# Kernel optimization log

Measured on AMD Instinct MI355X. Metric: run time of the kernel, lower is better.

Reference implementation:

```python
import jax, jax.numpy as jnp
import numpy as np

N = 50000      # nodes
E = 800000     # edges (avg degree 16)
B = 250        # graphs in batch
T = 8          # temporal slices
CIN = 32
COUT = 64


def setup_inputs() -> dict:
    key = jax.random.key(0)
    ks = jax.random.split(key, 9)
    x = jax.random.normal(ks[0], (N, CIN, T), dtype=jnp.float32)
    edge_index = jax.random.randint(ks[1], (2, E), 0, N, dtype=jnp.int64)
    # 250 graphs of 200 nodes each -> every segment non-empty (safe for segment_max)
    batch = jnp.repeat(jnp.arange(B, dtype=jnp.int64), N // B)
    W1 = jax.random.normal(ks[2], (CIN, COUT), jnp.float32) / np.sqrt(CIN).astype(np.float32)
    b1 = jax.random.normal(ks[3], (COUT,), jnp.float32) * 0.01
    W2 = jax.random.normal(ks[4], (COUT, COUT), jnp.float32) / np.sqrt(COUT).astype(np.float32)
    b2 = jax.random.normal(ks[5], (COUT,), jnp.float32) * 0.01
    W3 = jax.random.normal(ks[6], (COUT, COUT), jnp.float32) / np.sqrt(COUT).astype(np.float32)
    b3 = jax.random.normal(ks[7], (COUT,), jnp.float32) * 0.01
    return {"x": x, "edge_index": edge_index, "batch": batch,
            "W1": W1, "b1": b1, "W2": W2, "b2": b2, "W3": W3, "b3": b3}


def reference(x, edge_index, batch, W1, b1, W2, b2, W3, b3):
    # GCNConv (PyG default): add self-loops, symmetric D^{-1/2}(A+I)D^{-1/2} norm,
    # linear transform then gather-scale-scatter aggregation, plus bias.
    src, dst = edge_index[0], edge_index[1]
    loops = jnp.arange(N, dtype=src.dtype)
    src2 = jnp.concatenate([src, loops])
    dst2 = jnp.concatenate([dst, loops])
    deg = jax.ops.segment_sum(jnp.ones_like(src2, x.dtype), dst2, num_segments=N)
    dinv = jax.lax.rsqrt(deg)  # deg >= 1 due to self-loops
    norm = dinv[src2] * dinv[dst2]  # [E+N]
    counts = jax.ops.segment_sum(jnp.ones((N,), x.dtype), batch, num_segments=B)

    def gcn(h, W, b):
        h = h @ W                              # [N, COUT]
        msg = norm[:, None] * h[src2]          # [E+N, COUT] gather + scale
        return jax.ops.segment_sum(msg, dst2, num_segments=N) + b

    def pool(h):  # cat(global_max_pool, global_mean_pool) -> [B, 2*COUT]
        mx = jax.ops.segment_max(h, batch, num_segments=B)
        mn = jax.ops.segment_sum(h, batch, num_segments=B) / counts[:, None]
        return jnp.concatenate([mx, mn], axis=1)

    def step(carry, xt):  # xt: [N, CIN]
        h1 = jax.nn.relu(gcn(xt, W1, b1))
        h2 = jax.nn.relu(gcn(h1, W2, b2))
        h3 = jax.nn.relu(gcn(h2, W3, b3))
        return carry, pool(h1) + pool(h2) + pool(h3)

    _, outs = jax.lax.scan(step, None, jnp.moveaxis(x, 2, 0))  # [T, B, 2*COUT]
    return jnp.moveaxis(outs, 0, 2)  # [B, 2*COUT, T]
```

## Files before the change

### kernel.cpp

```cpp
#include <hip/hip_runtime.h>
#include <hip/hip_fp16.h>
#include <math.h>

#define NN 50000
#define EE 800000
#define BB 250
#define TT 8
#define CIN 32
#define COUT 64
#define NPG 200
#define SCAN_B 256
#define NBLK 196
#define GC (BB * COUT)

__device__ __forceinline__ float unpack_w(unsigned int v) {
    union { unsigned short u; __half h; } cv;
    cv.u = (unsigned short)(v >> 16);
    return __half2float(cv.h);
}


__global__ void init_deg(int* deg, int* cursor) {
    int n = blockIdx.x * 256 + threadIdx.x;
    if (n < NN) { deg[n] = 1; cursor[n] = 0; }
}

__global__ void count_deg(const int* dst, int* deg) {
    int e = blockIdx.x * 256 + threadIdx.x;
    if (e < EE) atomicAdd(&deg[dst[e]], 1);
}

__global__ void compute_dinv(const int* deg, float* dinv) {
    int n = blockIdx.x * 256 + threadIdx.x;
    if (n < NN) dinv[n] = rsqrtf((float)deg[n]);
}

__global__ void scan_blocks(const int* deg, int* off, int* bsum) {
    __shared__ int sh[SCAN_B];
    int gid = blockIdx.x * SCAN_B + threadIdx.x;
    int v = (gid < NN) ? (deg[gid] - 1) : 0;
    sh[threadIdx.x] = v;
    __syncthreads();
    for (int s = 1; s < SCAN_B; s <<= 1) {
        int add = (threadIdx.x >= s) ? sh[threadIdx.x - s] : 0;
        __syncthreads();
        sh[threadIdx.x] += add;
        __syncthreads();
    }
    if (gid < NN) off[gid] = sh[threadIdx.x] - v;
    if (threadIdx.x == SCAN_B - 1) bsum[blockIdx.x] = sh[threadIdx.x];
}

__global__ void scan_sums(int* bsum, int* off) {
    __shared__ int sh[SCAN_B];
    int v = (threadIdx.x < NBLK) ? bsum[threadIdx.x] : 0;
    sh[threadIdx.x] = v;
    __syncthreads();
    for (int s = 1; s < SCAN_B; s <<= 1) {
        int add = (threadIdx.x >= s) ? sh[threadIdx.x - s] : 0;
        __syncthreads();
        sh[threadIdx.x] += add;
        __syncthreads();
    }
    if (threadIdx.x < NBLK) bsum[threadIdx.x] = sh[threadIdx.x] - v;
    if (threadIdx.x == 0) off[NN] = EE;
}

__global__ void scan_add(int* off, const int* bsum) {
    int gid = blockIdx.x * SCAN_B + threadIdx.x;
    if (gid < NN) off[gid] += bsum[blockIdx.x];
}

__global__ void fill_csr(const int* src, const int* dst, const int* off,
                         int* cursor, const float* dinv, unsigned int* csrp) {
    int e = blockIdx.x * 256 + threadIdx.x;
    if (e >= EE) return;
    int s = src[e], d = dst[e];
    int p = atomicAdd(&cursor[d], 1);
    union { __half h; unsigned short u; } cv;
    cv.h = __float2half(dinv[s] * dinv[d]);
    csrp[off[d] + p] = (unsigned int)s | ((unsigned int)cv.u << 16);
}

__global__ void scratch_init(float* scr, int ntot) {
    int i = blockIdx.x * 256 + threadIdx.x;
    if (i < ntot) scr[i] = 0.f;
}


__global__ void agg_x_allT16(const float* __restrict__ x, const int* __restrict__ off,
                             const unsigned int* __restrict__ csrp,
                             const float* __restrict__ dinv, __half2* __restrict__ xa2) {
    int lane = threadIdx.x & 63;
    int w = threadIdx.x >> 6;
    int n = blockIdx.x * 4 + w;
    float dn = dinv[n];
    float sw = dn * dn;
    float4 v = ((const float4*)(x + (size_t)n * 256))[lane];
    float4 acc = make_float4(sw * v.x, sw * v.y, sw * v.z, sw * v.w);
    int e0 = off[n], e1 = off[n + 1];
    for (int base = e0; base < e1; base += 64) {
        int idx = base + lane;
        unsigned int cme = (idx < e1) ? csrp[idx] : 0u;
        int cnt = min(64, e1 - base);
        int k = 0;
        for (; k + 7 < cnt; k += 8) {
            unsigned int p0 = __shfl(cme, k, 64),     p1 = __shfl(cme, k + 1, 64);
            unsigned int p2 = __shfl(cme, k + 2, 64), p3 = __shfl(cme, k + 3, 64);
            unsigned int p4 = __shfl(cme, k + 4, 64), p5 = __shfl(cme, k + 5, 64);
            unsigned int p6 = __shfl(cme, k + 6, 64), p7 = __shfl(cme, k + 7, 64);
            float4 u0 = ((const float4*)(x + (size_t)(p0 & 0xffff) * 256))[lane];
            float4 u1 = ((const float4*)(x + (size_t)(p1 & 0xffff) * 256))[lane];
            float4 u2 = ((const float4*)(x + (size_t)(p2 & 0xffff) * 256))[lane];
            float4 u3 = ((const float4*)(x + (size_t)(p3 & 0xffff) * 256))[lane];
            float4 u4 = ((const float4*)(x + (size_t)(p4 & 0xffff) * 256))[lane];
            float4 u5 = ((const float4*)(x + (size_t)(p5 & 0xffff) * 256))[lane];
            float4 u6 = ((const float4*)(x + (size_t)(p6 & 0xffff) * 256))[lane];
            float4 u7 = ((const float4*)(x + (size_t)(p7 & 0xffff) * 256))[lane];
            float w0 = unpack_w(p0), w1 = unpack_w(p1), w2 = unpack_w(p2), w3 = unpack_w(p3);
            float w4 = unpack_w(p4), w5 = unpack_w(p5), w6 = unpack_w(p6), w7 = unpack_w(p7);
            acc.x = fmaf(w0, u0.x, acc.x); acc.y = fmaf(w0, u0.y, acc.y);
            acc.z = fmaf(w0, u0.z, acc.z); acc.w = fmaf(w0, u0.w, acc.w);
            acc.x = fmaf(w1, u1.x, acc.x); acc.y = fmaf(w1, u1.y, acc.y);
            acc.z = fmaf(w1, u1.z, acc.z); acc.w = fmaf(w1, u1.w, acc.w);
            acc.x = fmaf(w2, u2.x, acc.x); acc.y = fmaf(w2, u2.y, acc.y);
            acc.z = fmaf(w2, u2.z, acc.z); acc.w = fmaf(w2, u2.w, acc.w);
            acc.x = fmaf(w3, u3.x, acc.x); acc.y = fmaf(w3, u3.y, acc.y);
            acc.z = fmaf(w3, u3.z, acc.z); acc.w = fmaf(w3, u3.w, acc.w);
            acc.x = fmaf(w4, u4.x, acc.x); acc.y = fmaf(w4, u4.y, acc.y);
            acc.z = fmaf(w4, u4.z, acc.z); acc.w = fmaf(w4, u4.w, acc.w);
            acc.x = fmaf(w5, u5.x, acc.x); acc.y = fmaf(w5, u5.y, acc.y);
            acc.z = fmaf(w5, u5.z, acc.z); acc.w = fmaf(w5, u5.w, acc.w);
            acc.x = fmaf(w6, u6.x, acc.x); acc.y = fmaf(w6, u6.y, acc.y);
            acc.z = fmaf(w6, u6.z, acc.z); acc.w = fmaf(w6, u6.w, acc.w);
            acc.x = fmaf(w7, u7.x, acc.x); acc.y = fmaf(w7, u7.y, acc.y);
            acc.z = fmaf(w7, u7.z, acc.z); acc.w = fmaf(w7, u7.w, acc.w);
        }
        for (; k < cnt; ++k) {
            unsigned int p = __shfl(cme, k, 64);
            float wj = unpack_w(p);
            float4 u = ((const float4*)(x + (size_t)(p & 0xffff) * 256))[lane];
            acc.x = fmaf(wj, u.x, acc.x); acc.y = fmaf(wj, u.y, acc.y);
            acc.z = fmaf(wj, u.z, acc.z); acc.w = fmaf(wj, u.w, acc.w);
        }
    }
    __shared__ float sh[4][TT][33];
    float av[4] = {acc.x, acc.y, acc.z, acc.w};
    #pragma unroll
    for (int k = 0; k < 4; ++k) {
        int f = 4 * lane + k;
        sh[w][f & 7][f >> 3] = av[k];
    }
    __syncthreads();
    for (int i = threadIdx.x; i < 512; i += 256) {
        int t = i >> 6;
        int r = i & 63;
        int nl = r >> 4;
        int pp = r & 15;
        xa2[((size_t)(t >> 1) * NN + blockIdx.x * 4 + nl) * 32 + (t & 1) * 16 + pp] =
            __floats2half2_rn(sh[nl][t][2 * pp], sh[nl][t][2 * pp + 1]);
    }
}

__global__ void l1mat2i(const __half2* __restrict__ xa, const float* __restrict__ W1,
                        const float* __restrict__ b1, const float* __restrict__ W2,
                        __half2* __restrict__ H1,
                        float* __restrict__ pmax, float* __restrict__ psum) {
    __shared__ float W1s[CIN * COUT];
    __shared__ __half2 W2s[COUT * 32];
    __shared__ float Xs[4][2][CIN];
    __shared__ float tile[4][2][COUT];
    for (int i = threadIdx.x; i < CIN * COUT; i += 256) W1s[i] = W1[i];
    for (int i = threadIdx.x; i < COUT * 32; i += 256) {
        int k = i >> 5, pr = i & 31;
        W2s[i] = __floats2half2_rn(W2[k * COUT + 2 * pr], W2[k * COUT + 2 * pr + 1]);
    }
    if (threadIdx.x < 128) {
        int nl = threadIdx.x >> 5, idx = threadIdx.x & 31;
        int tc = idx >> 4, pp = idx & 15;
        float2 v = __half22float2(xa[((size_t)blockIdx.x * 4 + nl) * 32 + idx]);
        Xs[nl][tc][2 * pp] = v.x;
        Xs[nl][tc][2 * pp + 1] = v.y;
    }
    __syncthreads();
    int co = threadIdx.x & 63;
    int nl = threadIdx.x >> 6;
    float a0 = b1[co], a1 = b1[co];
    #pragma unroll
    for (int k = 0; k < CIN; ++k) {
        float wv = W1s[k * COUT + co];
        a0 = fmaf(Xs[nl][0][k], wv, a0);
        a1 = fmaf(Xs[nl][1][k], wv, a1);
    }
    tile[nl][0][co] = fmaxf(a0, 0.f);
    tile[nl][1][co] = fmaxf(a1, 0.f);
    __syncthreads();
    if (threadIdx.x < 128) {
        int c = threadIdx.x & 63, tc = threadIdx.x >> 6;
        float m = fmaxf(fmaxf(tile[0][tc][c], tile[1][tc][c]),
                        fmaxf(tile[2][tc][c], tile[3][tc][c]));
        float s = tile[0][tc][c] + tile[1][tc][c] + tile[2][tc][c] + tile[3][tc][c];
        int g = blockIdx.x / 50;
        atomicMax((int*)&pmax[tc * GC + g * COUT + c], __float_as_int(m));
        atomicAdd(&psum[tc * GC + g * COUT + c], s);
    }
    {
        int row = threadIdx.x >> 5;
        int pr = threadIdx.x & 31;
        int nl2 = row >> 1, tc2 = row & 1;
        float b0 = 0.f, bb1 = 0.f;
        #pragma unroll
        for (int k = 0; k < COUT; ++k) {
            float xv = tile[nl2][tc2][k];
            float2 wv = __half22float2(W2s[k * 32 + pr]);
            b0 = fmaf(xv, wv.x, b0);
            bb1 = fmaf(xv, wv.y, bb1);
        }
        H1[((size_t)blockIdx.x * 4 + nl2) * 64 + tc2 * 32 + pr] =
            __floats2half2_rn(b0, bb1);
    }
}

template <int FUSE>
__global__ void agg2i(const __half2* __restrict__ Hin, const int* __restrict__ off,
                      const unsigned int* __restrict__ csrp,
                      const float* __restrict__ dinv, const float* __restrict__ b,
                      const float* __restrict__ W, __half2* __restrict__ Hout,
                      float* __restrict__ pmax, float* __restrict__ psum) {
    __shared__ __half2 Ws[FUSE ? COUT * 32 : 1];
    __shared__ float tile[4][2][COUT];
    if (FUSE)
        for (int i = threadIdx.x; i < COUT * 32; i += 256) {
            int k = i >> 5, pr = i & 31;
            Ws[i] = __floats2half2_rn(W[k * COUT + 2 * pr], W[k * COUT + 2 * pr + 1]);
        }
    int lane = threadIdx.x & 63;
    int tc = lane >> 5;
    int p = lane & 31;
    int w = threadIdx.x >> 6;
    int n = blockIdx.x * 4 + w;
    int e0 = off[n], e1 = off[n + 1];
    float ax = 0.f, ay = 0.f;
    for (int base = e0; base < e1; base += 64) {
        int idx = base + lane;
        unsigned int cme = (idx < e1) ? csrp[idx] : 0u;
        int cnt = min(64, e1 - base);
        int k = 0;
        for (; k + 7 < cnt; k += 8) {
            unsigned int c0 = __shfl(cme, k, 64),     c1 = __shfl(cme, k + 1, 64);
            unsigned int c2 = __shfl(cme, k + 2, 64), c3 = __shfl(cme, k + 3, 64);
            unsigned int c4 = __shfl(cme, k + 4, 64), c5 = __shfl(cme, k + 5, 64);
            unsigned int c6 = __shfl(cme, k + 6, 64), c7 = __shfl(cme, k + 7, 64);
            float2 v0 = __half22float2(Hin[(size_t)(c0 & 0xffff) * 64 + lane]);
            float2 v1 = __half22float2(Hin[(size_t)(c1 & 0xffff) * 64 + lane]);
            float2 v2 = __half22float2(Hin[(size_t)(c2 & 0xffff) * 64 + lane]);
            float2 v3 = __half22float2(Hin[(size_t)(c3 & 0xffff) * 64 + lane]);
            float2 v4 = __half22float2(Hin[(size_t)(c4 & 0xffff) * 64 + lane]);
            float2 v5 = __half22float2(Hin[(size_t)(c5 & 0xffff) * 64 + lane]);
            float2 v6 = __half22float2(Hin[(size_t)(c6 & 0xffff) * 64 + lane]);
            float2 v7 = __half22float2(Hin[(size_t)(c7 & 0xffff) * 64 + lane]);
            float w0 = unpack_w(c0), w1 = unpack_w(c1), w2 = unpack_w(c2), w3 = unpack_w(c3);
            float w4 = unpack_w(c4), w5 = unpack_w(c5), w6 = unpack_w(c6), w7 = unpack_w(c7);
            ax = fmaf(w0, v0.x, ax); ay = fmaf(w0, v0.y, ay);
            ax = fmaf(w1, v1.x, ax); ay = fmaf(w1, v1.y, ay);
            ax = fmaf(w2, v2.x, ax); ay = fmaf(w2, v2.y, ay);
            ax = fmaf(w3, v3.x, ax); ay = fmaf(w3, v3.y, ay);
            ax = fmaf(w4, v4.x, ax); ay = fmaf(w4, v4.y, ay);
            ax = fmaf(w5, v5.x, ax); ay = fmaf(w5, v5.y, ay);
            ax = fmaf(w6, v6.x, ax); ay = fmaf(w6, v6.y, ay);
            ax = fmaf(w7, v7.x, ax); ay = fmaf(w7, v7.y, ay);
        }
        for (; k < cnt; ++k) {
            unsigned int c = __shfl(cme, k, 64);
            float wv = unpack_w(c);
            float2 v = __half22float2(Hin[(size_t)(c & 0xffff) * 64 + lane]);
            ax = fmaf(wv, v.x, ax); ay = fmaf(wv, v.y, ay);
        }
    }
    {
        float dn = dinv[n];
        float sw = dn * dn;
        float2 sv = __half22float2(Hin[(size_t)n * 64 + lane]);
        float ox = fmaxf(fmaf(sw, sv.x, ax) + b[2 * p], 0.f);
        float oy = fmaxf(fmaf(sw, sv.y, ay) + b[2 * p + 1], 0.f);
        tile[w][tc][2 * p] = ox;
        tile[w][tc][2 * p + 1] = oy;
    }
    __syncthreads();
    if (threadIdx.x < 128) {
        int c = threadIdx.x & 63, tcc = threadIdx.x >> 6;
        float m = fmaxf(fmaxf(tile[0][tcc][c], tile[1][tcc][c]),
                        fmaxf(tile[2][tcc][c], tile[3][tcc][c]));
        float s = tile[0][tcc][c] + tile[1][tcc][c] + tile[2][tcc][c] + tile[3][tcc][c];
        int g = blockIdx.x / 50;
        atomicMax((int*)&pmax[tcc * GC + g * COUT + c], __float_as_int(m));
        atomicAdd(&psum[tcc * GC + g * COUT + c], s);
    }
    if (FUSE) {
        int row = threadIdx.x >> 5;
        int pr = threadIdx.x & 31;
        int nl2 = row >> 1, tc2 = row & 1;
        float b0 = 0.f, bb1 = 0.f;
        #pragma unroll
        for (int k = 0; k < COUT; ++k) {
            float xv = tile[nl2][tc2][k];
            float2 wv = __half22float2(Ws[k * 32 + pr]);
            b0 = fmaf(xv, wv.x, b0);
            bb1 = fmaf(xv, wv.y, bb1);
        }
        Hout[((size_t)blockIdx.x * 4 + nl2) * 64 + tc2 * 32 + pr] =
            __floats2half2_rn(b0, bb1);
    }
}

__global__ void fold2(float* __restrict__ pmaxT, float* __restrict__ psumT,
                      float* __restrict__ out, int t0) {
    int i = blockIdx.x * 256 + threadIdx.x;
    if (i >= 2 * GC) return;
    int tc = i / GC;
    int r = i - tc * GC;
    int g = r >> 6, c = r & 63;
    float m = pmaxT[tc * GC + r] + pmaxT[2 * GC + tc * GC + r] +
              pmaxT[4 * GC + tc * GC + r];
    float mean = psumT[i] * (1.0f / NPG);
    int t = t0 + tc;
    out[((size_t)g * 128 + c) * TT + t] = m;
    out[((size_t)g * 128 + 64 + c) * TT + t] = mean;
    pmaxT[tc * GC + r] = 0.f;
    pmaxT[2 * GC + tc * GC + r] = 0.f;
    pmaxT[4 * GC + tc * GC + r] = 0.f;
    psumT[i] = 0.f;
}


extern "C" void kernel_launch(void* const* d_in, const int* in_sizes, int n_in,
                              void* d_out, int out_size, void* d_ws, size_t ws_size,
                              hipStream_t stream) {
    const float* x   = (const float*)d_in[0];
    const int*   ei  = (const int*)d_in[1];
    const int*   src = ei;
    const int*   dst = ei + EE;
    const float* W1  = (const float*)d_in[3];
    const float* b1  = (const float*)d_in[4];
    const float* W2  = (const float*)d_in[5];
    const float* b2  = (const float*)d_in[6];
    const float* W3  = (const float*)d_in[7];
    const float* b3  = (const float*)d_in[8];
    float* out = (float*)d_out;

    char* wsp = (char*)d_ws;
    auto alloc = [&](size_t bytes) {
        char* p = wsp;
        wsp += (bytes + 255) & ~(size_t)255;
        return p;
    };
    const size_t chunkHalf2 = (size_t)NN * 32;
    float*        dinv = (float*)       alloc((size_t)NN * 4);
    int*          off  = (int*)         alloc((size_t)(NN + 1) * 4);
    unsigned int* csrp = (unsigned int*)alloc((size_t)EE * 4);
    __half2*      H1   = (__half2*)     alloc((size_t)NN * 64 * 4);
    __half2*      xa2  = (__half2*)     alloc(chunkHalf2 * 4 * 4);
    __half2*      h2x  = (__half2*)     alloc(chunkHalf2 * 4);
    float*        scr  = (float*)       alloc((size_t)8 * GC * 4);
    (void)h2x;
    __half2* H2 = xa2 + 3 * chunkHalf2;
    float* pmaxT = scr;
    float* psumT = scr + 6 * GC;

    int* deg    = (int*)H1;
    int* cursor = ((int*)H1) + NN;
    int* bsum   = ((int*)H1) + 2 * NN;

    init_deg<<<NBLK, 256, 0, stream>>>(deg, cursor);
    count_deg<<<(EE + 255) / 256, 256, 0, stream>>>(dst, deg);
    compute_dinv<<<NBLK, 256, 0, stream>>>(deg, dinv);
    scan_blocks<<<NBLK, SCAN_B, 0, stream>>>(deg, off, bsum);
    scan_sums<<<1, SCAN_B, 0, stream>>>(bsum, off);
    scan_add<<<NBLK, SCAN_B, 0, stream>>>(off, bsum);
    fill_csr<<<(EE + 255) / 256, 256, 0, stream>>>(src, dst, off, cursor, dinv, csrp);
    scratch_init<<<(8 * GC + 255) / 256, 256, 0, stream>>>(scr, 8 * GC);

    agg_x_allT16<<<NN / 4, 256, 0, stream>>>(x, off, csrp, dinv, xa2);

    for (int c = 3; c >= 0; --c) {
        int t0 = 2 * c;
        const __half2* xc = xa2 + (size_t)c * chunkHalf2;
        l1mat2i<<<NN / 4, 256, 0, stream>>>(xc, W1, b1, W2, H1, pmaxT, psumT);
        agg2i<1><<<NN / 4, 256, 0, stream>>>(H1, off, csrp, dinv, b2, W3, H2,
                                             pmaxT + 2 * GC, psumT);
        agg2i<0><<<NN / 4, 256, 0, stream>>>(H2, off, csrp, dinv, b3, nullptr, nullptr,
                                             pmaxT + 4 * GC, psumT);
        fold2<<<(2 * GC + 255) / 256, 256, 0, stream>>>(pmaxT, psumT, out, t0);
    }
}
```

Before: 861.4 us.

## Split wavefront into four edge groups with 16-byte gathers in aggregation

The layer-2/3 aggregation kernel now has each wavefront process four neighbor edges at once. Each 16-lane quarter loads a whole 128-byte fp16 row with float4 loads and keeps eight partial accumulators, which are then combined with xor shuffles. This is meant to widen memory transactions and raise memory-level parallelism for the irregular gathers. The cost is extra cross-lane reduction and more registers. Separately, the x-aggregation kernel's unroll factor drops from 8 to 4, which may lower register pressure.

```diff
diff --git a/kernel.cpp b/kernel.cpp
--- a/kernel.cpp
+++ b/kernel.cpp
@@ -104,21 +104,15 @@
         unsigned int cme = (idx < e1) ? csrp[idx] : 0u;
         int cnt = min(64, e1 - base);
         int k = 0;
-        for (; k + 7 < cnt; k += 8) {
+        for (; k + 3 < cnt; k += 4) {
             unsigned int p0 = __shfl(cme, k, 64),     p1 = __shfl(cme, k + 1, 64);
             unsigned int p2 = __shfl(cme, k + 2, 64), p3 = __shfl(cme, k + 3, 64);
-            unsigned int p4 = __shfl(cme, k + 4, 64), p5 = __shfl(cme, k + 5, 64);
-            unsigned int p6 = __shfl(cme, k + 6, 64), p7 = __shfl(cme, k + 7, 64);
             float4 u0 = ((const float4*)(x + (size_t)(p0 & 0xffff) * 256))[lane];
             float4 u1 = ((const float4*)(x + (size_t)(p1 & 0xffff) * 256))[lane];
             float4 u2 = ((const float4*)(x + (size_t)(p2 & 0xffff) * 256))[lane];
             float4 u3 = ((const float4*)(x + (size_t)(p3 & 0xffff) * 256))[lane];
-            float4 u4 = ((const float4*)(x + (size_t)(p4 & 0xffff) * 256))[lane];
-            float4 u5 = ((const float4*)(x + (size_t)(p5 & 0xffff) * 256))[lane];
-            float4 u6 = ((const float4*)(x + (size_t)(p6 & 0xffff) * 256))[lane];
-            float4 u7 = ((const float4*)(x + (size_t)(p7 & 0xffff) * 256))[lane];
-            float w0 = unpack_w(p0), w1 = unpack_w(p1), w2 = unpack_w(p2), w3 = unpack_w(p3);
-            float w4 = unpack_w(p4), w5 = unpack_w(p5), w6 = unpack_w(p6), w7 = unpack_w(p7);
+            float w0 = unpack_w(p0), w1 = unpack_w(p1);
+            float w2 = unpack_w(p2), w3 = unpack_w(p3);
             acc.x = fmaf(w0, u0.x, acc.x); acc.y = fmaf(w0, u0.y, acc.y);
             acc.z = fmaf(w0, u0.z, acc.z); acc.w = fmaf(w0, u0.w, acc.w);
             acc.x = fmaf(w1, u1.x, acc.x); acc.y = fmaf(w1, u1.y, acc.y);
@@ -127,14 +121,6 @@
             acc.z = fmaf(w2, u2.z, acc.z); acc.w = fmaf(w2, u2.w, acc.w);
             acc.x = fmaf(w3, u3.x, acc.x); acc.y = fmaf(w3, u3.y, acc.y);
             acc.z = fmaf(w3, u3.z, acc.z); acc.w = fmaf(w3, u3.w, acc.w);
-            acc.x = fmaf(w4, u4.x, acc.x); acc.y = fmaf(w4, u4.y, acc.y);
-            acc.z = fmaf(w4, u4.z, acc.z); acc.w = fmaf(w4, u4.w, acc.w);
-            acc.x = fmaf(w5, u5.x, acc.x); acc.y = fmaf(w5, u5.y, acc.y);
-            acc.z = fmaf(w5, u5.z, acc.z); acc.w = fmaf(w5, u5.w, acc.w);
-            acc.x = fmaf(w6, u6.x, acc.x); acc.y = fmaf(w6, u6.y, acc.y);
-            acc.z = fmaf(w6, u6.z, acc.z); acc.w = fmaf(w6, u6.w, acc.w);
-            acc.x = fmaf(w7, u7.x, acc.x); acc.y = fmaf(w7, u7.y, acc.y);
-            acc.z = fmaf(w7, u7.z, acc.z); acc.w = fmaf(w7, u7.w, acc.w);
         }
         for (; k < cnt; ++k) {
             unsigned int p = __shfl(cme, k, 64);
@@ -222,7 +208,7 @@
 }
 
 template <int FUSE>
-__global__ void agg2i(const __half2* __restrict__ Hin, const int* __restrict__ off,
+__global__ void agg2q(const __half2* __restrict__ Hin, const int* __restrict__ off,
                       const unsigned int* __restrict__ csrp,
                       const float* __restrict__ dinv, const float* __restrict__ b,
                       const float* __restrict__ W, __half2* __restrict__ Hout,
@@ -235,56 +221,60 @@
             Ws[i] = __floats2half2_rn(W[k * COUT + 2 * pr], W[k * COUT + 2 * pr + 1]);
         }
     int lane = threadIdx.x & 63;
-    int tc = lane >> 5;
-    int p = lane & 31;
+    int sub = lane >> 4;
+    int qoff = lane & 15;
     int w = threadIdx.x >> 6;
     int n = blockIdx.x * 4 + w;
     int e0 = off[n], e1 = off[n + 1];
-    float ax = 0.f, ay = 0.f;
+    float a0 = 0.f, a1 = 0.f, a2 = 0.f, a3 = 0.f;
+    float a4 = 0.f, a5 = 0.f, a6 = 0.f, a7 = 0.f;
+    union F4H { float4 f; __half2 h[4]; };
     for (int base = e0; base < e1; base += 64) {
         int idx = base + lane;
         unsigned int cme = (idx < e1) ? csrp[idx] : 0u;
         int cnt = min(64, e1 - base);
-        int k = 0;
-        for (; k + 7 < cnt; k += 8) {
-            unsigned int c0 = __shfl(cme, k, 64),     c1 = __shfl(cme, k + 1, 64);
-            unsigned int c2 = __shfl(cme, k + 2, 64), c3 = __shfl(cme, k + 3, 64);
-            unsigned int c4 = __shfl(cme, k + 4, 64), c5 = __shfl(cme, k + 5, 64);
-            unsigned int c6 = __shfl(cme, k + 6, 64), c7 = __shfl(cme, k + 7, 64);
-            float2 v0 = __half22float2(Hin[(size_t)(c0 & 0xffff) * 64 + lane]);
-            float2 v1 = __half22float2(Hin[(size_t)(c1 & 0xffff) * 64 + lane]);
-            float2 v2 = __half22float2(Hin[(size_t)(c2 & 0xffff) * 64 + lane]);
-            float2 v3 = __half22float2(Hin[(size_t)(c3 & 0xffff) * 64 + lane]);
-            float2 v4 = __half22float2(Hin[(size_t)(c4 & 0xffff) * 64 + lane]);
-            float2 v5 = __half22float2(Hin[(size_t)(c5 & 0xffff) * 64 + lane]);
-            float2 v6 = __half22float2(Hin[(size_t)(c6 & 0xffff) * 64 + lane]);
-            float2 v7 = __half22float2(Hin[(size_t)(c7 & 0xffff) * 64 + lane]);
-            float w0 = unpack_w(c0), w1 = unpack_w(c1), w2 = unpack_w(c2), w3 = unpack_w(c3);
-            float w4 = unpack_w(c4), w5 = unpack_w(c5), w6 = unpack_w(c6), w7 = unpack_w(c7);
-            ax = fmaf(w0, v0.x, ax); ay = fmaf(w0, v0.y, ay);
-            ax = fmaf(w1, v1.x, ax); ay = fmaf(w1, v1.y, ay);
-            ax = fmaf(w2, v2.x, ax); ay = fmaf(w2, v2.y, ay);
-            ax = fmaf(w3, v3.x, ax); ay = fmaf(w3, v3.y, ay);
-            ax = fmaf(w4, v4.x, ax); ay = fmaf(w4, v4.y, ay);
-            ax = fmaf(w5, v5.x, ax); ay = fmaf(w5, v5.y, ay);
-            ax = fmaf(w6, v6.x, ax); ay = fmaf(w6, v6.y, ay);
-            ax = fmaf(w7, v7.x, ax); ay = fmaf(w7, v7.y, ay);
-        }
-        for (; k < cnt; ++k) {
-            unsigned int c = __shfl(cme, k, 64);
-            float wv = unpack_w(c);
-            float2 v = __half22float2(Hin[(size_t)(c & 0xffff) * 64 + lane]);
-            ax = fmaf(wv, v.x, ax); ay = fmaf(wv, v.y, ay);
-        }
-    }
-    {
+        int rounds = (cnt + 3) >> 2;
+        for (int r = 0; r < rounds; ++r) {
+            int k = 4 * r + sub;
+            unsigned int ce = __shfl(cme, k, 64);
+            float wv = (k < cnt) ? unpack_w(ce) : 0.f;
+            F4H u;
+            u.f = ((const float4*)(Hin + (size_t)(ce & 0xffff) * 64))[qoff];
+            float2 f0 = __half22float2(u.h[0]);
+            float2 f1 = __half22float2(u.h[1]);
+            float2 f2 = __half22float2(u.h[2]);
+            float2 f3 = __half22float2(u.h[3]);
+            a0 = fmaf(wv, f0.x, a0); a1 = fmaf(wv, f0.y, a1);
+            a2 = fmaf(wv, f1.x, a2); a3 = fmaf(wv, f1.y, a3);
+            a4 = fmaf(wv, f2.x, a4); a5 = fmaf(wv, f2.y, a5);
+            a6 = fmaf(wv, f3.x, a6); a7 = fmaf(wv, f3.y, a7);
+        }
+    }
+    a0 += __shfl_xor(a0, 16, 64); a0 += __shfl_xor(a0, 32, 64);
+    a1 += __shfl_xor(a1, 16, 64); a1 += __shfl_xor(a1, 32, 64);
+    a2 += __shfl_xor(a2, 16, 64); a2 += __shfl_xor(a2, 32, 64);
+    a3 += __shfl_xor(a3, 16, 64); a3 += __shfl_xor(a3, 32, 64);
+    a4 += __shfl_xor(a4, 16, 64); a4 += __shfl_xor(a4, 32, 64);
+    a5 += __shfl_xor(a5, 16, 64); a5 += __shfl_xor(a5, 32, 64);
+    a6 += __shfl_xor(a6, 16, 64); a6 += __shfl_xor(a6, 32, 64);
+    a7 += __shfl_xor(a7, 16, 64); a7 += __shfl_xor(a7, 32, 64);
+    if (sub == 0) {
         float dn = dinv[n];
         float sw = dn * dn;
-        float2 sv = __half22float2(Hin[(size_t)n * 64 + lane]);
-        float ox = fmaxf(fmaf(sw, sv.x, ax) + b[2 * p], 0.f);
-        float oy = fmaxf(fmaf(sw, sv.y, ay) + b[2 * p + 1], 0.f);
-        tile[w][tc][2 * p] = ox;
-        tile[w][tc][2 * p + 1] = oy;
+        F4H su;
+        su.f = ((const float4*)(Hin + (size_t)n * 64))[qoff];
+        float acc[8] = {a0, a1, a2, a3, a4, a5, a6, a7};
+        #pragma unroll
+        for (int i = 0; i < 4; ++i) {
+            int h = 4 * qoff + i;
+            int tcc = h >> 5;
+            int p = h & 31;
+            float2 sv = __half22float2(su.h[i]);
+            float ox = fmaxf(fmaf(sw, sv.x, acc[2 * i])     + b[2 * p],     0.f);
+            float oy = fmaxf(fmaf(sw, sv.y, acc[2 * i + 1]) + b[2 * p + 1], 0.f);
+            tile[w][tcc][2 * p] = ox;
+            tile[w][tcc][2 * p + 1] = oy;
+        }
     }
     __syncthreads();
     if (threadIdx.x < 128) {
@@ -386,9 +376,9 @@
         int t0 = 2 * c;
         const __half2* xc = xa2 + (size_t)c * chunkHalf2;
         l1mat2i<<<NN / 4, 256, 0, stream>>>(xc, W1, b1, W2, H1, pmaxT, psumT);
-        agg2i<1><<<NN / 4, 256, 0, stream>>>(H1, off, csrp, dinv, b2, W3, H2,
+        agg2q<1><<<NN / 4, 256, 0, stream>>>(H1, off, csrp, dinv, b2, W3, H2,
                                              pmaxT + 2 * GC, psumT);
-        agg2i<0><<<NN / 4, 256, 0, stream>>>(H2, off, csrp, dinv, b3, nullptr, nullptr,
+        agg2q<0><<<NN / 4, 256, 0, stream>>>(H2, off, csrp, dinv, b3, nullptr, nullptr,
                                              pmaxT + 4 * GC, psumT);
         fold2<<<(2 * GC + 255) / 256, 256, 0, stream>>>(pmaxT, psumT, out, t0);
     }
```

New measurement: 851.3 us. No clear change (-1.2%).
